# Optimization experiments

Hardware: AMD Instinct MI355X
Metric: run time of the kernel (lower is better)

Reference implementation:

```python
import jax, jax.numpy as jnp
import numpy as np

B, C, H, W = 32, 256, 32, 32
N_EMBED = 8192
BETA = 0.25  # used for the (unreturned) commitment loss in the original


def setup_inputs() -> dict:
    key = jax.random.key(0)
    k1, k2 = jax.random.split(key)
    z = jax.random.normal(k1, (B, C, H, W), dtype=jnp.float32)
    embedding = jax.random.normal(k2, (N_EMBED, C), dtype=jnp.float32)
    return {"z": z, "embedding": embedding}


def reference(z, embedding):
    # z: [b, c, h, w] -> [b, h, w, c] -> [N, d]
    b, c, h, w = z.shape
    z_bhwc = jnp.transpose(z, (0, 2, 3, 1))
    z_flat = z_bhwc.reshape(-1, c)  # [N, d]

    # Squared L2 distance to every codebook entry: [N, n_embed]
    d = (
        jnp.sum(z_flat * z_flat, axis=1, keepdims=True)
        + jnp.sum(embedding * embedding, axis=1)
        - 2.0 * jnp.einsum("nd,kd->nk", z_flat, embedding)
    )
    min_encoding_indices = jnp.argmin(d, axis=1)  # [N] int

    # Codebook gather + straight-through estimator
    z_q = embedding[min_encoding_indices].reshape(b, h, w, c)
    z_q = z_bhwc + jax.lax.stop_gradient(z_q - z_bhwc)
    z_q = jnp.transpose(z_q, (0, 3, 1, 2))  # back to [b, c, h, w]
    return z_q, min_encoding_indices
```

## Files before the change

### kernel.cpp

```cpp
#include <hip/hip_runtime.h>

#define BATCH   32
#define CDIM    256
#define HWSZ    1024
#define NTOK    32768
#define KEMB    8192
#define ZQ_SIZE (BATCH * CDIM * HWSZ)

typedef short bf16x8 __attribute__((ext_vector_type(8)));
typedef float floatx4 __attribute__((ext_vector_type(4)));

#define MSPLIT 4
#define STRIP  (KEMB / MSPLIT)
#define MB8    128
#define NB8    128
#define MT8    (STRIP / MB8)

#define WS8_ESQ   0ULL
#define WS8_EQM   32768ULL
#define WS8_EH    65536ULL
#define WS8_ZH    4259840ULL
#define WS8_ZL    21037056ULL
#define WS8_PART  37814272ULL
#define WS8_IDX   39911424ULL
#define WS8_TOTAL 40042496ULL

__device__ __forceinline__ unsigned short bf16rne(float f) {
    unsigned int u = __float_as_uint(f);
    return (unsigned short)((u + 0x7fffu + ((u >> 16) & 1u)) >> 16);
}
__device__ __forceinline__ unsigned int packsplit(float f) {
    unsigned int u  = __float_as_uint(f);
    unsigned int hi = (u + 0x7fffu + ((u >> 16) & 1u)) >> 16;
    float rest      = f - __uint_as_float(hi << 16);
    unsigned int u2 = __float_as_uint(rest);
    unsigned int lo = (u2 + 0x7fffu + ((u2 >> 16) & 1u)) >> 16;
    return (hi << 16) | lo;
}
__device__ __forceinline__ unsigned umin32(unsigned a, unsigned b) { return a < b ? a : b; }
__device__ __forceinline__ unsigned umax32(unsigned a, unsigned b) { return a > b ? a : b; }

#define GLOAD_LDS16(g, l) \
    __builtin_amdgcn_global_load_lds((const __attribute__((address_space(1))) void*)(g), \
                                     (__attribute__((address_space(3))) void*)(l), 16, 0, 0)

__global__ void esqcvt_kernel(const float* __restrict__ emb, float* __restrict__ eSq,
                              float* __restrict__ eqm, unsigned short* __restrict__ eh) {
    int k    = blockIdx.x * 4 + (threadIdx.x >> 6);
    int lane = threadIdx.x & 63;
    float4 v = *(const float4*)&emb[k * CDIM + lane * 4];
    float s  = v.x * v.x + v.y * v.y + v.z * v.z + v.w * v.w;
    #pragma unroll
    for (int off = 32; off; off >>= 1) s += __shfl_down(s, off);
    ushort4 h = make_ushort4(bf16rne(v.x), bf16rne(v.y), bf16rne(v.z), bf16rne(v.w));
    *(ushort4*)&eh[k * CDIM + lane * 4] = h;
    if (lane == 0) { eSq[k] = s; eqm[k] = s * 2048.0f + 8388608.0f; }
}

__global__ void splitz_kernel(const float* __restrict__ z, unsigned short* __restrict__ zh,
                              unsigned short* __restrict__ zl) {
    __shared__ unsigned int tile[64][65];
    int b  = blockIdx.x >> 6;
    int r  = blockIdx.x & 63;
    int dt = r >> 4, ht = r & 15;
    int t  = threadIdx.x;
    #pragma unroll
    for (int i = 0; i < 4; ++i) {
        int u  = t + 256 * i;
        int dr = u >> 4;
        int c4 = (u & 15) * 4;
        float4 v = *(const float4*)&z[(((size_t)(b * 256 + dt * 64 + dr)) << 10) + ht * 64 + c4];
        tile[dr][c4 + 0] = packsplit(v.x);
        tile[dr][c4 + 1] = packsplit(v.y);
        tile[dr][c4 + 2] = packsplit(v.z);
        tile[dr][c4 + 3] = packsplit(v.w);
    }
    __syncthreads();
    #pragma unroll
    for (int i = 0; i < 2; ++i) {
        int u  = t + 256 * i;
        int tr = u & 63;
        int d8 = u >> 6;
        unsigned short h8[8], l8[8];
        #pragma unroll
        for (int j = 0; j < 8; ++j) {
            unsigned int p = tile[d8 * 8 + j][tr];
            h8[j] = (unsigned short)(p >> 16);
            l8[j] = (unsigned short)(p & 0xffff);
        }
        size_t off = (size_t)(b * 1024 + ht * 64 + tr) * 256 + dt * 64 + d8 * 8;
        *(uint4*)&zh[off] = *(uint4*)h8;
        *(uint4*)&zl[off] = *(uint4*)l8;
    }
}

__global__ __launch_bounds__(256, 2)
void dist8_kernel(const unsigned short* __restrict__ zhp,
                  const unsigned short* __restrict__ ehp,
                  const float* __restrict__ eqm,
                  uint4* __restrict__ part) {
    __shared__ __align__(16) char lds[65536];

    const int t    = threadIdx.x;
    const int lane = t & 63;
    const int wv   = t >> 6;
    const int wm   = wv >> 1, wn = wv & 1;
    const int l15  = lane & 15, quad = lane >> 4;

    const int nb = blockIdx.x & 255;
    const int q  = blockIdx.x >> 8;
    const int n0 = nb * NB8;
    const int cstrip = q * STRIP;

    const int dmaRow  = lane >> 3;
    const int dmaChnk = (lane & 7) ^ dmaRow;
    const unsigned laneGoff = (unsigned)dmaRow * 512 + (unsigned)dmaChnk * 16;

    const char* gA0 = (const char*)ehp + (size_t)(cstrip + wv * 32) * 512 + laneGoff;
    const char* gB0 = (const char*)zhp + (size_t)(n0 + wv * 32) * 512 + laneGoff;
    const unsigned wvOff = (unsigned)wv * 4096;

    unsigned aR[4], bR[4];
    #pragma unroll
    for (int rf = 0; rf < 4; ++rf) aR[rf] = (unsigned)(wm * 64 + rf * 16 + l15) * 128;
    #pragma unroll
    for (int cf = 0; cf < 4; ++cf) bR[cf] = 16384u + (unsigned)(wn * 64 + cf * 16 + l15) * 128;
    const unsigned cx = (unsigned)(l15 & 7);

    unsigned k1[4], k2[4], k3[4];
    #pragma unroll
    for (int cf = 0; cf < 4; ++cf) { k1[cf] = 0xFFFFFFFFu; k2[cf] = 0xFFFFFFFFu; k3[cf] = 0xFFFFFFFFu; }

    #pragma unroll
    for (int j = 0; j < 4; ++j) {
        GLOAD_LDS16(gA0 + j * 4096, lds + wvOff + j * 1024);
        GLOAD_LDS16(gB0 + j * 4096, lds + 16384u + wvOff + j * 1024);
    }

    int r = 0;
    for (int mt = 0; mt < MT8; ++mt) {
        floatx4 acc[4][4];
        #pragma unroll
        for (int rf = 0; rf < 4; ++rf)
            #pragma unroll
            for (int cf = 0; cf < 4; ++cf) acc[rf][cf] = (floatx4){0.f, 0.f, 0.f, 0.f};

        #pragma unroll
        for (int dr = 0; dr < 4; ++dr, ++r) {
            __syncthreads();
            if (r + 1 < 4 * MT8) {
                const int rn  = r + 1;
                const int mtn = rn >> 2, drn = rn & 3;
                const unsigned bon = (unsigned)(rn & 1) << 15;
                const char* ga = gA0 + (size_t)mtn * 65536 + drn * 128;
                const char* gb = gB0 + drn * 128;
                #pragma unroll
                for (int j = 0; j < 4; ++j) {
                    GLOAD_LDS16(ga + j * 4096, lds + bon + wvOff + j * 1024);
                    GLOAD_LDS16(gb + j * 4096, lds + bon + 16384u + wvOff + j * 1024);
                }
            }
            const unsigned bo = (unsigned)(r & 1) << 15;
            #pragma unroll
            for (int dk = 0; dk < 2; ++dk) {
                const unsigned xoff = bo + (((unsigned)(dk * 4) + (unsigned)quad) ^ cx) * 16;
                bf16x8 bfr[4], afr[4];
                #pragma unroll
                for (int cf = 0; cf < 4; ++cf) bfr[cf] = *(const bf16x8*)(lds + bR[cf] + xoff);
                #pragma unroll
                for (int rf = 0; rf < 4; ++rf) afr[rf] = *(const bf16x8*)(lds + aR[rf] + xoff);
                #pragma unroll
                for (int rf = 0; rf < 4; ++rf)
                    #pragma unroll
                    for (int cf = 0; cf < 4; ++cf)
                        acc[rf][cf] = __builtin_amdgcn_mfma_f32_16x16x32_bf16(afr[rf], bfr[cf], acc[rf][cf], 0, 0, 0);
            }
        }

        #pragma unroll
        for (int rf = 0; rf < 4; ++rf) {
            const int kb = cstrip + mt * MB8 + wm * 64 + rf * 16 + quad * 4;
            floatx4 eq = *(const floatx4*)&eqm[kb];
            const unsigned lb = (unsigned)(mt * MB8 + wm * 64 + rf * 16 + quad * 4);
            #pragma unroll
            for (int cf = 0; cf < 4; ++cf) {
                #pragma unroll
                for (int rr = 0; rr < 4; ++rr) {
                    float kf = fmaf(acc[rf][cf][rr], -4096.f, eq[rr]);
                    unsigned key = (__float_as_uint(kf) << 11) | (lb + (unsigned)rr);
                    unsigned m1 = umax32(k1[cf], key);
                    k1[cf] = umin32(k1[cf], key);
                    unsigned m2 = umax32(k2[cf], m1);
                    k2[cf] = umin32(k2[cf], m1);
                    k3[cf] = umin32(k3[cf], m2);
                }
            }
        }
    }

    #pragma unroll
    for (int cf = 0; cf < 4; ++cf) {
        #pragma unroll
        for (int s = 0; s < 2; ++s) {
            int m = s ? 32 : 16;
            unsigned o1 = (unsigned)__shfl((int)k1[cf], lane ^ m, 64);
            unsigned o2 = (unsigned)__shfl((int)k2[cf], lane ^ m, 64);
            unsigned o3 = (unsigned)__shfl((int)k3[cf], lane ^ m, 64);
            unsigned a1  = umax32(k1[cf], o1);
            k1[cf]       = umin32(k1[cf], o1);
            unsigned b1  = umin32(k2[cf], o2);
            unsigned r3a = umax32(a1, b1);
            k2[cf]       = umin32(a1, b1);
            k3[cf]       = umin32(r3a, umin32(k3[cf], o3));
        }
    }

    __syncthreads();
    uint4* red = (uint4*)lds;
    if (quad == 0) {
        #pragma unroll
        for (int cf = 0; cf < 4; ++cf)
            red[wm * 128 + wn * 64 + cf * 16 + l15] = make_uint4(k1[cf], k2[cf], k3[cf], 0u);
    }
    __syncthreads();
    if (t < 128) {
        uint4 a = red[t], b = red[128 + t];
        unsigned a1  = umax32(a.x, b.x);
        unsigned r1  = umin32(a.x, b.x);
        unsigned b1  = umin32(a.y, b.y);
        unsigned r3a = umax32(a1, b1);
        unsigned r2  = umin32(a1, b1);
        unsigned r3  = umin32(r3a, umin32(a.z, b.z));
        part[q * NTOK + n0 + t] = make_uint4(r1, r2, r3, 0u);
    }
}

__global__ void rescore12_kernel(const unsigned short* __restrict__ zh,
                                 const unsigned short* __restrict__ zl,
                                 const float* __restrict__ emb,
                                 const float* __restrict__ eSq, const uint4* __restrict__ part,
                                 int* __restrict__ idx, float* __restrict__ idxF) {
    int n    = blockIdx.x * 4 + (threadIdx.x >> 6);
    int lane = threadIdx.x & 63;
    int c[12];
    #pragma unroll
    for (int s = 0; s < 4; ++s) {
        uint4 p = part[s * NTOK + n];
        c[3 * s]     = s * STRIP + (int)(p.x & 0x7FFu);
        c[3 * s + 1] = s * STRIP + (int)(p.y & 0x7FFu);
        c[3 * s + 2] = s * STRIP + (int)(p.z & 0x7FFu);
    }
    ushort4 h = *(const ushort4*)&zh[(size_t)n * CDIM + lane * 4];
    ushort4 l = *(const ushort4*)&zl[(size_t)n * CDIM + lane * 4];
    float z0 = __uint_as_float((unsigned)h.x << 16) + __uint_as_float((unsigned)l.x << 16);
    float z1 = __uint_as_float((unsigned)h.y << 16) + __uint_as_float((unsigned)l.y << 16);
    float z2 = __uint_as_float((unsigned)h.z << 16) + __uint_as_float((unsigned)l.z << 16);
    float z3 = __uint_as_float((unsigned)h.w << 16) + __uint_as_float((unsigned)l.w << 16);
    float acc[12];
    #pragma unroll
    for (int s = 0; s < 12; ++s) {
        float4 e = *(const float4*)&emb[(size_t)c[s] * CDIM + lane * 4];
        acc[s] = fmaf(z0, e.x, fmaf(z1, e.y, fmaf(z2, e.z, z3 * e.w)));
    }
    #pragma unroll
    for (int off = 32; off; off >>= 1) {
        #pragma unroll
        for (int s = 0; s < 12; ++s) acc[s] += __shfl_down(acc[s], off);
    }
    if (lane == 0) {
        float bd = 3.4e38f; int bi = 0x7fffffff;
        #pragma unroll
        for (int s = 0; s < 12; ++s) {
            float dv = eSq[c[s]] - 2.f * acc[s];
            if (dv < bd || (dv == bd && c[s] < bi)) { bd = dv; bi = c[s]; }
        }
        idx[n]  = bi;
        idxF[n] = (float)bi;
    }
}

__global__ void gather2_kernel(const float* __restrict__ emb, const int* __restrict__ idx,
                               float* __restrict__ out) {
    __shared__ float tile[32 * 260];
    __shared__ int rows[32];
    const int t  = threadIdx.x;
    const int n0 = blockIdx.x * 32;
    if (t < 32) rows[t] = idx[n0 + t];
    __syncthreads();
    {
        int r  = t >> 3;
        int c0 = (t & 7) * 32;
        const float* src = emb + (size_t)rows[r] * CDIM + c0;
        #pragma unroll
        for (int j = 0; j < 8; ++j) {
            float4 v = *(const float4*)(src + j * 4);
            *(float4*)&tile[r * 260 + c0 + j * 4] = v;
        }
    }
    __syncthreads();
    const int b   = n0 >> 10;
    const int hw0 = n0 & 1023;
    const int cg  = t >> 3;
    const int h4  = (t & 7) * 4;
    #pragma unroll
    for (int j = 0; j < 8; ++j) {
        int c = cg + j * 32;
        float4 v;
        v.x = tile[(h4 + 0) * 260 + c];
        v.y = tile[(h4 + 1) * 260 + c];
        v.z = tile[(h4 + 2) * 260 + c];
        v.w = tile[(h4 + 3) * 260 + c];
        *(float4*)&out[((size_t)b << 18) | ((size_t)c << 10) | (size_t)(hw0 + h4)] = v;
    }
}

#define F_BM  128
#define F_BK  128
#define F_BD  32
#define F_BSS (F_BK + 4)
#define F_KSPLIT 4
#define F_KPER  (KEMB / F_KSPLIT)
#define FWS_ESQ 0
#define FWS_PV  32768
#define FWS_PI  557056
#define FWS_IDX 1081344

__global__ void esq_kernel(const float* __restrict__ emb, float* __restrict__ eSq) {
    int k    = blockIdx.x * 4 + (threadIdx.x >> 6);
    int lane = threadIdx.x & 63;
    float4 v = *(const float4*)&emb[k * CDIM + lane * 4];
    float s  = v.x * v.x + v.y * v.y + v.z * v.z + v.w * v.w;
    #pragma unroll
    for (int off = 32; off; off >>= 1) s += __shfl_down(s, off);
    if (lane == 0) eSq[k] = s;
}

__global__ void dist_kernel(const float* __restrict__ z, const float* __restrict__ emb,
                            const float* __restrict__ eSq,
                            float* __restrict__ pv, int* __restrict__ pi) {
    __shared__ __align__(16) char smem[(F_BD * F_BM + F_BD * F_BSS) * 4];
    float (*As)[F_BM]  = (float (*)[F_BM])smem;
    float (*Bs)[F_BSS] = (float (*)[F_BSS])(smem + F_BD * F_BM * 4);
    const int t = threadIdx.x, tx = t & 15, ty = t >> 4;
    const int rb = blockIdx.x & 255, q = blockIdx.x >> 8;
    const int m0 = rb * F_BM, bb = m0 >> 10, hw0 = m0 & 1023;
    float minv[8]; int mini[8];
    #pragma unroll
    for (int i = 0; i < 8; ++i) { minv[i] = 3.4028235e38f; mini[i] = 0; }
    const int kbeg = q * F_KPER;
    for (int k0 = kbeg; k0 < kbeg + F_KPER; k0 += F_BK) {
        float acc[8][8];
        #pragma unroll
        for (int r = 0; r < 8; ++r)
            #pragma unroll
            for (int c = 0; c < 8; ++c) acc[r][c] = 0.f;
        for (int d0 = 0; d0 < CDIM; d0 += F_BD) {
            __syncthreads();
            #pragma unroll
            for (int i = 0; i < 4; ++i) {
                int u = t + i * 256; int m4 = (u & 31) << 2; int cR = u >> 5;
                float4 v = *(const float4*)&z[(bb << 18) + ((d0 + cR) << 10) + hw0 + m4];
                *(float4*)&As[cR][m4] = v;
            }
            #pragma unroll
            for (int i = 0; i < 4; ++i) {
                int u = t + i * 256; int kR = u >> 3; int c4 = (u & 7) << 2;
                float4 v = *(const float4*)&emb[(k0 + kR) * CDIM + d0 + c4];
                Bs[c4 + 0][kR] = v.x; Bs[c4 + 1][kR] = v.y;
                Bs[c4 + 2][kR] = v.z; Bs[c4 + 3][kR] = v.w;
            }
            __syncthreads();
            #pragma unroll
            for (int d = 0; d < F_BD; ++d) {
                float a[8], bb2[8];
                *(float4*)&a[0] = *(const float4*)&As[d][(ty << 2)];
                *(float4*)&a[4] = *(const float4*)&As[d][64 + (ty << 2)];
                *(float4*)&bb2[0] = *(const float4*)&Bs[d][(tx << 2)];
                *(float4*)&bb2[4] = *(const float4*)&Bs[d][64 + (tx << 2)];
                #pragma unroll
                for (int r = 0; r < 8; ++r)
                    #pragma unroll
                    for (int c = 0; c < 8; ++c) acc[r][c] = fmaf(a[r], bb2[c], acc[r][c]);
            }
        }
        #pragma unroll
        for (int c = 0; c < 8; ++c) {
            int kk = (c < 4) ? ((tx << 2) + c) : (64 + (tx << 2) + (c - 4));
            int kg = k0 + kk;
            float es = eSq[kg];
            #pragma unroll
            for (int r = 0; r < 8; ++r) {
                float v = fmaf(-2.f, acc[r][c], es);
                if (v < minv[r]) { minv[r] = v; mini[r] = kg; }
            }
        }
    }
    __syncthreads();
    float (*redV)[16] = (float (*)[16])smem;
    int   (*redI)[16] = (int   (*)[16])(smem + F_BM * 16 * 4);
    #pragma unroll
    for (int r = 0; r < 8; ++r) {
        int row = (r < 4) ? ((ty << 2) + r) : (64 + (ty << 2) + (r - 4));
        redV[row][tx] = minv[r]; redI[row][tx] = mini[r];
    }
    __syncthreads();
    if (t < F_BM) {
        float bv = redV[t][0]; int bi = redI[t][0];
        #pragma unroll
        for (int i = 1; i < 16; ++i) {
            float v = redV[t][i]; int ii = redI[t][i];
            if (v < bv || (v == bv && ii < bi)) { bv = v; bi = ii; }
        }
        int n = m0 + t;
        pv[q * NTOK + n] = bv; pi[q * NTOK + n] = bi;
    }
}

__global__ void merge_kernel(const float* __restrict__ pv, const int* __restrict__ pi,
                             int* __restrict__ idxOut, float* __restrict__ idxFOut) {
    int n = blockIdx.x * 256 + threadIdx.x;
    float bv = pv[n]; int bi = pi[n];
    #pragma unroll
    for (int q = 1; q < F_KSPLIT; ++q) {
        float v = pv[q * NTOK + n]; int ii = pi[q * NTOK + n];
        if (v < bv || (v == bv && ii < bi)) { bv = v; bi = ii; }
    }
    idxOut[n] = bi; idxFOut[n] = (float)bi;
}

extern "C" void kernel_launch(void* const* d_in, const int* in_sizes, int n_in,
                              void* d_out, int out_size, void* d_ws, size_t ws_size,
                              hipStream_t stream) {
    const float* z   = (const float*)d_in[0];
    const float* emb = (const float*)d_in[1];
    float* out = (float*)d_out;
    char*  ws  = (char*)d_ws;

    if (ws_size >= WS8_TOTAL) {
        float*          eSq  = (float*)(ws + WS8_ESQ);
        float*          eqm  = (float*)(ws + WS8_EQM);
        unsigned short* eh   = (unsigned short*)(ws + WS8_EH);
        unsigned short* zh   = (unsigned short*)(ws + WS8_ZH);
        unsigned short* zl   = (unsigned short*)(ws + WS8_ZL);
        uint4*          part = (uint4*)(ws + WS8_PART);
        int*            idx  = (int*)(ws + WS8_IDX);

        esqcvt_kernel <<<KEMB / 4, 256, 0, stream>>>(emb, eSq, eqm, eh);
        splitz_kernel <<<2048, 256, 0, stream>>>(z, zh, zl);
        dist8_kernel  <<<256 * MSPLIT, 256, 0, stream>>>(zh, eh, eqm, part);
        rescore12_kernel<<<NTOK / 4, 256, 0, stream>>>(zh, zl, emb, eSq, part, idx, out + ZQ_SIZE);
        gather2_kernel<<<NTOK / 32, 256, 0, stream>>>(emb, idx, out);
    } else {
        float* eSq = (float*)(ws + FWS_ESQ);
        float* pv  = (float*)(ws + FWS_PV);
        int*   pi  = (int*)(ws + FWS_PI);
        int*   idx = (int*)(ws + FWS_IDX);
        esq_kernel  <<<KEMB / 4, 256, 0, stream>>>(emb, eSq);
        dist_kernel <<<256 * F_KSPLIT, 256, 0, stream>>>(z, emb, eSq, pv, pi);
        merge_kernel<<<NTOK / 256, 256, 0, stream>>>(pv, pi, idx, out + ZQ_SIZE);
        gather2_kernel<<<NTOK / 32, 256, 0, stream>>>(emb, idx, out);
    }
}
```

Before: 309.1 us.

## Keep z tile fragments resident in registers across all codebook tiles

```diff
diff --git a/kernel.cpp b/kernel.cpp
--- a/kernel.cpp
+++ b/kernel.cpp
@@ -119,23 +119,39 @@
     const char* gA0 = (const char*)ehp + (size_t)(cstrip + wv * 32) * 512 + laneGoff;
     const char* gB0 = (const char*)zhp + (size_t)(n0 + wv * 32) * 512 + laneGoff;
     const unsigned wvOff = (unsigned)wv * 4096;
-
-    unsigned aR[4], bR[4];
+    const unsigned cx = (unsigned)(l15 & 7);
+
+    #pragma unroll
+    for (int dr = 0; dr < 4; ++dr)
+        #pragma unroll
+        for (int j = 0; j < 4; ++j)
+            GLOAD_LDS16(gB0 + dr * 128 + j * 4096, lds + dr * 16384 + wvOff + j * 1024);
+    __syncthreads();
+
+    bf16x8 bfr[4][4][2];
+    #pragma unroll
+    for (int cf = 0; cf < 4; ++cf) {
+        const unsigned bRow = (unsigned)(wn * 64 + cf * 16 + l15) * 128;
+        #pragma unroll
+        for (int dr = 0; dr < 4; ++dr)
+            #pragma unroll
+            for (int dk = 0; dk < 2; ++dk)
+                bfr[cf][dr][dk] = *(const bf16x8*)(lds + (unsigned)dr * 16384 + bRow +
+                                    (((unsigned)(dk * 4) + (unsigned)quad) ^ cx) * 16);
+    }
+    __syncthreads();
+
+    unsigned aR[4];
     #pragma unroll
     for (int rf = 0; rf < 4; ++rf) aR[rf] = (unsigned)(wm * 64 + rf * 16 + l15) * 128;
-    #pragma unroll
-    for (int cf = 0; cf < 4; ++cf) bR[cf] = 16384u + (unsigned)(wn * 64 + cf * 16 + l15) * 128;
-    const unsigned cx = (unsigned)(l15 & 7);
 
     unsigned k1[4], k2[4], k3[4];
     #pragma unroll
     for (int cf = 0; cf < 4; ++cf) { k1[cf] = 0xFFFFFFFFu; k2[cf] = 0xFFFFFFFFu; k3[cf] = 0xFFFFFFFFu; }
 
     #pragma unroll
-    for (int j = 0; j < 4; ++j) {
+    for (int j = 0; j < 4; ++j)
         GLOAD_LDS16(gA0 + j * 4096, lds + wvOff + j * 1024);
-        GLOAD_LDS16(gB0 + j * 4096, lds + 16384u + wvOff + j * 1024);
-    }
 
     int r = 0;
     for (int mt = 0; mt < MT8; ++mt) {
@@ -151,29 +167,24 @@
             if (r + 1 < 4 * MT8) {
                 const int rn  = r + 1;
                 const int mtn = rn >> 2, drn = rn & 3;
-                const unsigned bon = (unsigned)(rn & 1) << 15;
+                const unsigned bon = (unsigned)(rn & 1) << 14;
                 const char* ga = gA0 + (size_t)mtn * 65536 + drn * 128;
-                const char* gb = gB0 + drn * 128;
                 #pragma unroll
-                for (int j = 0; j < 4; ++j) {
+                for (int j = 0; j < 4; ++j)
                     GLOAD_LDS16(ga + j * 4096, lds + bon + wvOff + j * 1024);
-                    GLOAD_LDS16(gb + j * 4096, lds + bon + 16384u + wvOff + j * 1024);
-                }
-            }
-            const unsigned bo = (unsigned)(r & 1) << 15;
+            }
+            const unsigned bo = (unsigned)(r & 1) << 14;
             #pragma unroll
             for (int dk = 0; dk < 2; ++dk) {
                 const unsigned xoff = bo + (((unsigned)(dk * 4) + (unsigned)quad) ^ cx) * 16;
-                bf16x8 bfr[4], afr[4];
-                #pragma unroll
-                for (int cf = 0; cf < 4; ++cf) bfr[cf] = *(const bf16x8*)(lds + bR[cf] + xoff);
+                bf16x8 afr[4];
                 #pragma unroll
                 for (int rf = 0; rf < 4; ++rf) afr[rf] = *(const bf16x8*)(lds + aR[rf] + xoff);
                 #pragma unroll
                 for (int rf = 0; rf < 4; ++rf)
                     #pragma unroll
                     for (int cf = 0; cf < 4; ++cf)
-                        acc[rf][cf] = __builtin_amdgcn_mfma_f32_16x16x32_bf16(afr[rf], bfr[cf], acc[rf][cf], 0, 0, 0);
+                        acc[rf][cf] = __builtin_amdgcn_mfma_f32_16x16x32_bf16(afr[rf], bfr[cf][dr][dk], acc[rf][cf], 0, 0, 0);
             }
         }
 
```

New measurement: 291.3 us. 5.8% less time.
